# Kernel optimization log

Hardware: AMD Instinct MI355X
Metric: run time of the kernel (lower is better)

## Reference

```python
import jax, jax.numpy as jnp
import numpy as np

B, D_IN, D_OUT, DICT = 2048, 768, 768, 24576
TOP_K, TOP_K_AUX = 32, 512
L1_COEFF, AUX_PENALTY, N_DEAD = 0.001, 0.03125, 100.0


def setup_inputs() -> dict:
    key = jax.random.key(0)
    k1, k2, k3, k4, k5, k6 = jax.random.split(key, 6)
    x_in = jax.random.normal(k1, (B, D_IN), dtype=jnp.float32)
    y_target = jax.random.normal(k2, (B, D_OUT), dtype=jnp.float32)
    nb = jax.random.randint(k3, (DICT,), 0, 200).astype(jnp.float32)
    # kaiming-uniform-ish init
    bound_e = float(np.sqrt(6.0 / D_IN))
    W_enc = jax.random.uniform(k4, (D_IN, DICT), minval=-bound_e, maxval=bound_e, dtype=jnp.float32)
    bound_d = float(np.sqrt(6.0 / DICT))
    W_dec = jax.random.uniform(k5, (DICT, D_OUT), minval=-bound_d, maxval=bound_d, dtype=jnp.float32)
    W_dec = W_dec / jnp.linalg.norm(W_dec, axis=-1, keepdims=True)  # unit-norm rows
    b_dec = jnp.zeros((D_OUT,), dtype=jnp.float32)
    return {"x_in": x_in, "y_target": y_target, "num_batches_not_active": nb,
            "W_enc": W_enc, "W_dec": W_dec, "b_dec": b_dec}


def _unit_norm(x):
    m = x.mean(axis=-1, keepdims=True)
    x = x - m
    s = jnp.std(x, axis=-1, keepdims=True, ddof=1)  # torch .std is unbiased
    return x / (s + 1e-5), m, s


def reference(x_in, y_target, num_batches_not_active, W_enc, W_dec, b_dec):
    xn, _, _ = _unit_norm(x_in)
    yn, y_mean, y_std = _unit_norm(y_target)
    x_enc = xn - b_dec  # pre_enc_bias (input_size == output_size)
    acts = jax.nn.relu(x_enc @ W_enc)                      # [B, DICT]
    vals, idx = jax.lax.top_k(acts, TOP_K)                 # [B, TOP_K]
    rows = jnp.arange(B)[:, None]
    acts_sparse = jnp.zeros_like(acts).at[rows, idx].set(vals)
    y_pred = acts_sparse @ W_dec + b_dec                   # [B, D_OUT]
    y_pred_out = y_pred * y_std + y_mean

    # stateful dead-feature bookkeeping (update_inactive_features)
    col_active = acts_sparse.sum(axis=0) > 0
    nb = jnp.where(col_active, 0.0, num_batches_not_active + 1.0)

    l2_loss = jnp.mean((y_pred - yn) ** 2)
    l1_norm = jnp.mean(jnp.abs(acts_sparse).sum(axis=-1))
    l1_loss = L1_COEFF * l1_norm
    l0_norm = jnp.mean((acts_sparse > 0).astype(jnp.float32).sum(axis=-1))

    # auxiliary loss on dead features (static-shape masked top-k; masked cols
    # get -1 < relu acts so extras relu-clip to 0 -> same math as torch gather)
    dead = nb >= N_DEAD
    masked = jnp.where(dead[None, :], acts, -1.0)
    av, ai = jax.lax.top_k(masked, TOP_K_AUX)
    av = jax.nn.relu(av)
    acts_aux = jnp.zeros_like(acts).at[rows, ai].set(av)
    y_pred_aux = acts_aux @ W_dec
    residual = yn - y_pred
    l2_aux = AUX_PENALTY * jnp.mean((y_pred_aux - residual) ** 2)
    aux_loss = jnp.where(dead.any(), l2_aux, 0.0)

    loss = l2_loss + l1_loss + aux_loss
    num_dead_features = (nb > N_DEAD).sum()
    return (y_pred_out, acts_sparse, loss, l2_loss, l1_loss, l0_norm, l1_norm,
            aux_loss, num_dead_features)
```

## Files before the change

### kernel.cpp

```cpp
#include <hip/hip_runtime.h>
#include <math.h>

#define BATCH 2048
#define DIN 768
#define DICT 24576
#define KM 32
#define KA 512
#define NPT 48
#define L1_COEFF 0.001f
#define AUX_PENALTY 0.03125f
#define CAND_MAX 128
#define CAND_DELTA 0.08f
#define AUX_SPLIT 8

typedef __attribute__((ext_vector_type(8))) short bf16x8;
typedef __attribute__((ext_vector_type(8))) unsigned short u16x8;
typedef __attribute__((ext_vector_type(4))) float f32x4;

constexpr size_t WS_XENC   = 0;
constexpr size_t WS_YN     = WS_XENC + (size_t)BATCH*DIN;
constexpr size_t WS_YMEAN  = WS_YN + (size_t)BATCH*DIN;
constexpr size_t WS_YSTD   = WS_YMEAN + BATCH;
constexpr size_t WS_RES    = WS_YSTD + BATCH;
constexpr size_t WS_NSEL   = WS_RES + (size_t)BATCH*DIN;
constexpr size_t WS_SEL    = WS_NSEL + BATCH;
constexpr size_t WS_SELV   = WS_SEL + (size_t)BATCH*KM;
constexpr size_t WS_COLACT = WS_SELV + (size_t)BATCH*KM;
constexpr size_t WS_ACC    = WS_COLACT + DICT;
constexpr size_t WS_DB     = WS_ACC + 8;
constexpr size_t WS_XEB    = WS_DB + DICT/32;
constexpr size_t WS_WETF   = WS_XEB + (size_t)BATCH*DIN/2;
constexpr size_t WS_WETB   = WS_WETF + (size_t)DICT*DIN;
constexpr size_t WS_WDB    = WS_WETB + (size_t)DICT*DIN/2;
constexpr size_t WS_DCNT   = WS_XEB;
constexpr size_t WS_DPREF  = WS_XEB + DICT/32;
constexpr size_t WS_META   = WS_XEB + 2*(DICT/32);

__device__ __forceinline__ unsigned short f2b(float f){
    unsigned u = __float_as_uint(f);
    return (unsigned short)((u + 0x7fffu + ((u >> 16) & 1u)) >> 16);
}
__device__ __forceinline__ float b2f(unsigned short h){ return __uint_as_float(((unsigned)h) << 16); }

__device__ __forceinline__ void gld_lds16(const void* g, void* l){
    __builtin_amdgcn_global_load_lds(
        (const __attribute__((address_space(1))) unsigned int*)g,
        (__attribute__((address_space(3))) unsigned int*)l, 16, 0, 0);
}

__device__ __forceinline__ int blk_count512_w(int cw, int* s16, int par){
    if ((threadIdx.x & 63) == 0) s16[par*8 + (threadIdx.x >> 6)] = cw;
    __syncthreads();
    int tot = 0;
    #pragma unroll
    for (int w=0; w<8; w++) tot += s16[par*8+w];
    return tot;
}
__device__ __forceinline__ float blk_sum512(float v, float* s16, int par){
    #pragma unroll
    for (int off=32; off; off>>=1) v += __shfl_down(v, off);
    if ((threadIdx.x & 63) == 0) s16[par*8 + (threadIdx.x >> 6)] = v;
    __syncthreads();
    float t = 0.f;
    #pragma unroll
    for (int w=0; w<8; w++) t += s16[par*8+w];
    return t;
}
__device__ __forceinline__ float blk_sum256(float v, float* s8, int par){
    #pragma unroll
    for (int off=32; off; off>>=1) v += __shfl_down(v, off);
    if ((threadIdx.x & 63) == 0) s8[par*4 + (threadIdx.x >> 6)] = v;
    __syncthreads();
    float t = 0.f;
    #pragma unroll
    for (int w=0; w<4; w++) t += s8[par*4+w];
    return t;
}

__global__ __launch_bounds__(256) void normalize_k(const float* __restrict__ x,
        const float* __restrict__ y, const float* __restrict__ bdec,
        float* __restrict__ ws){
    __shared__ float s8[8];
    int b = blockIdx.x; bool isy = b >= BATCH; int row = isy ? b - BATCH : b;
    const float* src = (isy ? y : x) + (size_t)row*DIN;
    int tid = threadIdx.x;
    float v0 = src[tid], v1 = src[tid+256], v2 = src[tid+512];
    float s = blk_sum256(v0+v1+v2, s8, 0);
    float mean = s * (1.f/(float)DIN);
    float d0 = v0-mean, d1 = v1-mean, d2 = v2-mean;
    float vs = blk_sum256(d0*d0+d1*d1+d2*d2, s8, 1);
    float sd = sqrtf(vs / (float)(DIN-1));
    float inv = 1.f / (sd + 1e-5f);
    if (isy){
        float* yn = ws + WS_YN + (size_t)row*DIN;
        yn[tid] = d0*inv; yn[tid+256] = d1*inv; yn[tid+512] = d2*inv;
        if (tid==0){ ws[WS_YMEAN+row] = mean; ws[WS_YSTD+row] = sd; }
    } else {
        float* xe = ws + WS_XENC + (size_t)row*DIN;
        unsigned short* xeb = (unsigned short*)(ws + WS_XEB) + (size_t)row*DIN;
        float e0 = d0*inv - bdec[tid];
        float e1 = d1*inv - bdec[tid+256];
        float e2 = d2*inv - bdec[tid+512];
        xe[tid] = e0; xe[tid+256] = e1; xe[tid+512] = e2;
        xeb[tid] = f2b(e0); xeb[tid+256] = f2b(e1); xeb[tid+512] = f2b(e2);
    }
}

__global__ __launch_bounds__(256) void transpose_k(const float* __restrict__ W,
        float* __restrict__ Tf, unsigned short* __restrict__ Tb){
    __shared__ float t[32][33];
    int n0 = blockIdx.x*32, k0 = blockIdx.y*32;
    int r = threadIdx.x >> 5, c = threadIdx.x & 31;
    #pragma unroll
    for (int rr=r; rr<32; rr+=8) t[rr][c] = W[(size_t)(k0+rr)*DICT + n0 + c];
    __syncthreads();
    #pragma unroll
    for (int rr=r; rr<32; rr+=8){
        float v = t[c][rr];
        Tf[(size_t)(n0+rr)*DIN + k0 + c] = v;
        Tb[(size_t)(n0+rr)*DIN + k0 + c] = f2b(v);
    }
}

__global__ __launch_bounds__(256) void wdect_k(const float* __restrict__ W,
        unsigned short* __restrict__ T){
    __shared__ float t[32][33];
    int j0 = blockIdx.x*32, n0 = blockIdx.y*32;
    int r = threadIdx.x >> 5, c = threadIdx.x & 31;
    #pragma unroll
    for (int rr=r; rr<32; rr+=8) t[rr][c] = W[(size_t)(j0+rr)*DIN + n0 + c];
    __syncthreads();
    #pragma unroll
    for (int rr=r; rr<32; rr+=8)
        T[(size_t)(n0+rr)*DICT + j0 + c] = f2b(t[c][rr]);
}

__global__ __launch_bounds__(256) void gemm_mfma(const unsigned short* __restrict__ Abf,
        const unsigned short* __restrict__ Bbf, unsigned short* __restrict__ C){
    __shared__ __align__(16) unsigned short As[128*64];
    __shared__ __align__(16) unsigned short Bs[128*64];
    const int tid = threadIdx.x;
    const int w = tid >> 6, lane = tid & 63;
    const int m0 = blockIdx.y*128, n0 = blockIdx.x*128;
    const int srow = lane >> 3;
    const int schunk = (lane & 7) ^ srow;
    const int wm = (w >> 1)*64, wn = (w & 1)*64;
    f32x4 acc[16];
    #pragma unroll
    for (int i=0;i<16;i++) acc[i] = (f32x4){0.f,0.f,0.f,0.f};
    for (int kt = 0; kt < DIN; kt += 64){
        #pragma unroll
        for (int q=0;q<4;q++){
            int s = w*4 + q;
            int row = 8*s + srow;
            gld_lds16(Abf + (size_t)(m0+row)*DIN + kt + schunk*8, &As[8*s*64]);
            gld_lds16(Bbf + (size_t)(n0+row)*DIN + kt + schunk*8, &Bs[8*s*64]);
        }
        __syncthreads();
        #pragma unroll
        for (int kk=0; kk<64; kk+=32){
            bf16x8 af[4], bfr[4];
            int ch = (kk>>3) + (lane>>4);
            #pragma unroll
            for (int i=0;i<4;i++){
                int row = wm + i*16 + (lane&15);
                af[i] = *(const bf16x8*)&As[row*64 + ((ch ^ (row&7))<<3)];
            }
            #pragma unroll
            for (int j=0;j<4;j++){
                int row = wn + j*16 + (lane&15);
                bfr[j] = *(const bf16x8*)&Bs[row*64 + ((ch ^ (row&7))<<3)];
            }
            #pragma unroll
            for (int i=0;i<4;i++)
                #pragma unroll
                for (int j=0;j<4;j++)
                    acc[i*4+j] = __builtin_amdgcn_mfma_f32_16x16x32_bf16(af[i], bfr[j], acc[i*4+j], 0,0,0);
        }
        __syncthreads();
    }
    #pragma unroll
    for (int i=0;i<4;i++){
        #pragma unroll
        for (int r=0;r<4;r++){
            int m = m0 + wm + i*16 + (lane>>4)*4 + r;
            unsigned short* crow = C + (size_t)m*DICT + n0 + wn + (lane&15);
            #pragma unroll
            for (int j=0;j<4;j++)
                crow[j*16] = f2b(fmaxf(acc[i*4+j][r], 0.f) + 0.0f);
        }
    }
}

__global__ __launch_bounds__(512) void topk_main(const unsigned short* __restrict__ actsb,
        const float* __restrict__ WeTf, const float* __restrict__ Wdec,
        const float* __restrict__ bdec, float* __restrict__ ws,
        float* __restrict__ ypred_out){
    const int row = blockIdx.x, tid = threadIdx.x;
    const int lane = tid & 63, wid = tid >> 6;
    __shared__ int   s_i16[16];
    __shared__ float s_f16[16];
    __shared__ float s_x[DIN];
    __shared__ int   s_ci[CAND_MAX];
    __shared__ float s_cv[CAND_MAX];
    __shared__ int   s_li[KM];
    __shared__ float s_lv[KM];
    __shared__ int   s_n, s_m;
    const unsigned short* arow = actsb + (size_t)row * DICT;
    const float* xrow = ws + WS_XENC + (size_t)row * DIN;
    unsigned short h[NPT];
    #pragma unroll
    for (int i=0;i<6;i++){
        u16x8 v = *(const u16x8*)&arow[i*4096 + tid*8];
        #pragma unroll
        for (int e=0;e<8;e++) h[i*8+e] = v[e];
    }
    s_x[tid] = xrow[tid];
    if (tid < DIN-512) s_x[tid+512] = xrow[tid+512];
    if (tid == 0){ s_n = 0; s_m = 0; }

    int par = 0;
    unsigned prefix = 0;
    for (int bit=14; bit>=0; bit--){
        unsigned cand = prefix | (1u<<bit);
        int c = 0;
        #pragma unroll
        for (int q=0;q<NPT;q++) c += (int)__popcll(__ballot((unsigned)h[q] >= cand));
        int tot = blk_count512_w(c, s_i16, par); par ^= 1;
        if (tot >= KM) prefix = cand;
    }
    float tc = b2f((unsigned short)prefix) - CAND_DELTA;
    #pragma unroll
    for (int q=0;q<NPT;q++){
        if (b2f(h[q]) > tc){
            int p = atomicAdd(&s_n, 1);
            if (p < CAND_MAX) s_ci[p] = (q>>3)*4096 + tid*8 + (q&7);
        }
    }
    __syncthreads();
    int nc = s_n; if (nc > CAND_MAX) nc = CAND_MAX;
    for (int c = wid; c < nc; c += 8){
        const float* wr = WeTf + (size_t)s_ci[c]*DIN;
        float p = 0.f;
        #pragma unroll
        for (int t=0; t<12; t++) p = fmaf(s_x[lane + 64*t], wr[lane + 64*t], p);
        #pragma unroll
        for (int off=32; off; off>>=1) p += __shfl_down(p, off);
        if (lane == 0) s_cv[c] = fmaxf(p, 0.f);
    }
    __syncthreads();
    if (tid < nc){
        float vi = s_cv[tid]; int ii = s_ci[tid];
        int rank = 0;
        for (int j=0; j<nc; j++){
            float vj = s_cv[j];
            rank += (vj > vi) || (vj == vi && s_ci[j] < ii);
        }
        if (rank < KM){
            int p = atomicAdd(&s_m, 1);
            s_li[p] = ii; s_lv[p] = vi;
        }
    }
    __syncthreads();
    if (tid < KM){
        ((int*)ws)[WS_COLACT + s_li[tid]] = 1;
        ((int*)ws)[WS_SEL  + (size_t)row*KM + tid] = s_li[tid];
        ws[WS_SELV + (size_t)row*KM + tid] = s_lv[tid];
    }
    if (tid == 0){
        float l1 = 0.f; int l0 = 0;
        for (int l=0;l<KM;l++){ l1 += s_lv[l]; l0 += (s_lv[l] > 0.f); }
        atomicAdd(&ws[WS_ACC+1], l1);
        atomicAdd(&ws[WS_ACC+2], (float)l0);
    }
    __syncthreads();
    float ym = ws[WS_YMEAN+row], ys = ws[WS_YSTD+row];
    float l2loc = 0.f;
    for (int c = tid; c < DIN; c += 512){
        float acc = bdec[c];
        #pragma unroll 4
        for (int l=0;l<KM;l++) acc = fmaf(s_lv[l], Wdec[(size_t)s_li[l]*DIN + c], acc);
        float ynv = ws[WS_YN + (size_t)row*DIN + c];
        float d = acc - ynv;
        l2loc += d*d;
        ws[WS_RES + (size_t)row*DIN + c] = ynv - acc;
        ypred_out[(size_t)row*DIN + c] = fmaf(acc, ys, ym);
    }
    float l2t = blk_sum512(l2loc, s_f16, 0);
    if (tid==0) atomicAdd(&ws[WS_ACC+0], l2t);
}

__global__ __launch_bounds__(256) void dead_update(const float* __restrict__ nb,
        float* __restrict__ ws){
    int j = blockIdx.x*256 + threadIdx.x;
    int lane = threadIdx.x & 63;
    int act = ((const int*)ws)[WS_COLACT + j];
    float nbn = act ? 0.f : nb[j] + 1.f;
    bool dead = nbn >= 100.0f;
    unsigned long long bal = __ballot(dead ? 1 : 0);
    if (lane == 0){
        unsigned* db = (unsigned*)(ws + WS_DB);
        int* dc = (int*)(ws + WS_DCNT);
        int w = j >> 5;
        db[w]   = (unsigned)bal;
        db[w+1] = (unsigned)(bal >> 32);
        dc[w]   = __popc((unsigned)bal);
        dc[w+1] = __popc((unsigned)(bal >> 32));
        if (bal) atomicOr(((int*)ws) + WS_ACC + 5, 1);
    }
    int c = (nbn > 100.0f) ? 1 : 0;
    #pragma unroll
    for (int off=32; off; off>>=1) c += __shfl_down(c, off);
    if (lane == 0 && c) atomicAdd(&ws[WS_ACC+4], (float)c);
}

__global__ __launch_bounds__(256) void scan_k(float* __restrict__ ws){
    __shared__ int s[DICT/32];
    const int* dc = (const int*)(ws + WS_DCNT);
    int tid = threadIdx.x;
    for (int i=tid; i<DICT/32; i+=256) s[i] = dc[i];
    __syncthreads();
    for (int off=1; off<DICT/32; off<<=1){
        int v[3];
        #pragma unroll
        for (int k=0;k<3;k++){ int i = tid + 256*k; v[k] = (i >= off) ? s[i-off] : 0; }
        __syncthreads();
        #pragma unroll
        for (int k=0;k<3;k++){ int i = tid + 256*k; s[i] += v[k]; }
        __syncthreads();
    }
    int* dp = (int*)(ws + WS_DPREF);
    for (int i=tid; i<DICT/32; i+=256) dp[i] = s[i] - dc[i];
    if (tid == 0){
        int nd = s[DICT/32 - 1];
        int ndpad = (nd + 63) & ~63;
        int nkt = ndpad >> 6;
        int* meta = (int*)(ws + WS_META);
        meta[0] = nd; meta[1] = ndpad; meta[2] = nkt;
        meta[3] = (nkt + AUX_SPLIT - 1) / AUX_SPLIT;
    }
}

__global__ __launch_bounds__(256) void wdtcompact_k(float* __restrict__ ws,
        unsigned short* __restrict__ wdt){
    __shared__ unsigned s_db[DICT/32];
    __shared__ int      s_dp[DICT/32];
    const int tid = threadIdx.x, n = blockIdx.x;
    for (int i=tid; i<DICT/32; i+=256){
        s_db[i] = ((const unsigned*)(ws + WS_DB))[i];
        s_dp[i] = ((const int*)(ws + WS_DPREF))[i];
    }
    const int nd    = ((const int*)(ws + WS_META))[0];
    const int ndpad = ((const int*)(ws + WS_META))[1];
    __syncthreads();
    unsigned short* row = wdt + (size_t)n*DICT;
    for (int ch = 0; ch < DICT; ch += 4096){
        unsigned short v[16];
        u16x8 a = *(const u16x8*)&row[ch + tid*16];
        u16x8 b = *(const u16x8*)&row[ch + tid*16 + 8];
        #pragma unroll
        for (int e=0;e<8;e++){ v[e] = a[e]; v[8+e] = b[e]; }
        __syncthreads();
        int w = (ch>>5) + (tid>>1);
        unsigned dbw = s_db[w]; int dpw = s_dp[w];
        int bit0 = (tid&1)*16;
        #pragma unroll
        for (int e=0;e<16;e++){
            int bit = bit0 + e;
            if ((dbw >> bit) & 1u)
                row[dpw + __popc(dbw & ((1u<<bit)-1u))] = v[e];
        }
        __syncthreads();
    }
    for (int t = nd + tid; t < ndpad; t += 256) row[t] = 0;
}

__global__ __launch_bounds__(512) void aux_select(unsigned short* __restrict__ actsb,
        float* __restrict__ ws){
    const int row = blockIdx.x, tid = threadIdx.x;
    __shared__ int      s_i16[16];
    __shared__ unsigned s_db[DICT/32];
    __shared__ int      s_dp[DICT/32];
    unsigned short* arow = actsb + (size_t)row * DICT;
    for (int i=tid; i<DICT/32; i+=512){
        s_db[i] = ((const unsigned*)(ws + WS_DB))[i];
        s_dp[i] = ((const int*)(ws + WS_DPREF))[i];
    }
    const int nd    = ((const int*)(ws + WS_META))[0];
    const int ndpad = ((const int*)(ws + WS_META))[1];
    __syncthreads();

    unsigned short key[NPT];
    #pragma unroll
    for (int i=0;i<6;i++){
        u16x8 v = *(const u16x8*)&arow[i*4096 + tid*8];
        unsigned dbw = s_db[i*128 + (tid>>2)];
        #pragma unroll
        for (int e=0;e<8;e++){
            unsigned short hv = v[e];
            key[i*8+e] = (((dbw >> ((tid&3)*8 + e)) & 1u) && hv) ? hv : 0;
        }
    }

    int par = 0;
    unsigned prefix = 0;
    for (int bit=14; bit>=0; bit--){
        unsigned cand = prefix | (1u<<bit);
        int c = 0;
        #pragma unroll
        for (int q=0;q<NPT;q++) c += (int)__popcll(__ballot((unsigned)key[q] >= cand));
        int tot = blk_count512_w(c, s_i16, par); par ^= 1;
        if (tot >= KA) prefix = cand;
    }
    unsigned thr = prefix ? prefix : 1u;

    #pragma unroll
    for (int i=0;i<6;i++){
        int w = i*128 + (tid>>2);
        unsigned dbw = s_db[w];
        int dpw = s_dp[w];
        #pragma unroll
        for (int e=0;e<8;e++){
            int bit = (tid&3)*8 + e;
            if ((dbw >> bit) & 1u){
                int p = dpw + __popc(dbw & ((1u<<bit)-1u));
                unsigned short kv = key[i*8+e];
                arow[p] = ((unsigned)kv >= thr) ? kv : (unsigned short)0;
            }
        }
    }
    for (int t = nd + tid; t < ndpad; t += 512) arow[t] = 0;
}

__global__ __launch_bounds__(256) void aux_gemm(const unsigned short* __restrict__ Abf,
        const unsigned short* __restrict__ Bbf, const float* __restrict__ ws,
        float* __restrict__ yaux){
    const int nkt   = ((const int*)(ws + WS_META))[2];
    const int chunk = ((const int*)(ws + WS_META))[3];
    int t0 = blockIdx.z * chunk;
    int t1 = t0 + chunk; if (t1 > nkt) t1 = nkt;
    if (t0 >= t1) return;
    __shared__ __align__(16) unsigned short As[128*64];
    __shared__ __align__(16) unsigned short Bs[128*64];
    const int tid = threadIdx.x;
    const int w = tid >> 6, lane = tid & 63;
    const int m0 = blockIdx.y*128, n0 = blockIdx.x*128;
    const int srow = lane >> 3;
    const int schunk = (lane & 7) ^ srow;
    const int wm = (w >> 1)*64, wn = (w & 1)*64;
    f32x4 acc[16];
    #pragma unroll
    for (int i=0;i<16;i++) acc[i] = (f32x4){0.f,0.f,0.f,0.f};
    for (int t = t0; t < t1; ++t){
        int kt = t*64;
        #pragma unroll
        for (int q=0;q<4;q++){
            int s = w*4 + q;
            int row = 8*s + srow;
            gld_lds16(Abf + (size_t)(m0+row)*DICT + kt + schunk*8, &As[8*s*64]);
            gld_lds16(Bbf + (size_t)(n0+row)*DICT + kt + schunk*8, &Bs[8*s*64]);
        }
        __syncthreads();
        #pragma unroll
        for (int kk=0; kk<64; kk+=32){
            bf16x8 af[4], bfr[4];
            int ch = (kk>>3) + (lane>>4);
            #pragma unroll
            for (int i=0;i<4;i++){
                int row = wm + i*16 + (lane&15);
                af[i] = *(const bf16x8*)&As[row*64 + ((ch ^ (row&7))<<3)];
            }
            #pragma unroll
            for (int j=0;j<4;j++){
                int row = wn + j*16 + (lane&15);
                bfr[j] = *(const bf16x8*)&Bs[row*64 + ((ch ^ (row&7))<<3)];
            }
            #pragma unroll
            for (int i=0;i<4;i++)
                #pragma unroll
                for (int j=0;j<4;j++)
                    acc[i*4+j] = __builtin_amdgcn_mfma_f32_16x16x32_bf16(af[i], bfr[j], acc[i*4+j], 0,0,0);
        }
        __syncthreads();
    }
    #pragma unroll
    for (int i=0;i<4;i++){
        #pragma unroll
        for (int r=0;r<4;r++){
            int m = m0 + wm + i*16 + (lane>>4)*4 + r;
            float* crow = yaux + (size_t)m*DIN + n0 + wn + (lane&15);
            #pragma unroll
            for (int j=0;j<4;j++) atomicAdd(&crow[j*16], acc[i*4+j][r]);
        }
    }
}

__global__ __launch_bounds__(256) void auxloss_k(const float* __restrict__ yaux,
        float* __restrict__ ws){
    __shared__ float s8[8];
    const float4* y4 = (const float4*)yaux;
    const float4* r4 = (const float4*)(ws + WS_RES);
    float s = 0.f;
    const size_t n4 = (size_t)BATCH*DIN/4;
    for (size_t i = (size_t)blockIdx.x*256 + threadIdx.x; i < n4; i += (size_t)gridDim.x*256){
        float4 a = y4[i], b = r4[i];
        float d0 = a.x-b.x, d1 = a.y-b.y, d2 = a.z-b.z, d3 = a.w-b.w;
        s += d0*d0 + d1*d1 + d2*d2 + d3*d3;
    }
    float tot = blk_sum256(s, s8, 0);
    if (threadIdx.x == 0) atomicAdd(&ws[WS_ACC+3], tot);
}

__global__ __launch_bounds__(256) void zscatter(const float* __restrict__ ws,
        float* __restrict__ acts){
    const int row = blockIdx.x, tid = threadIdx.x;
    float4 z = make_float4(0.f,0.f,0.f,0.f);
    float4* arow4 = (float4*)(acts + (size_t)row*DICT);
    #pragma unroll
    for (int i=0;i<24;i++) arow4[tid + 256*i] = z;
    __syncthreads();
    if (tid < KM){
        int j   = ((const int*)ws)[WS_SEL + (size_t)row*KM + tid];
        float v = ws[WS_SELV + (size_t)row*KM + tid];
        (acts + (size_t)row*DICT)[j] = v;
    }
}

__global__ void finalize_k(const float* __restrict__ ws, float* __restrict__ out){
    if (threadIdx.x == 0){
        float l2   = ws[WS_ACC+0] / (float)((size_t)BATCH*DIN);
        float l1n  = ws[WS_ACC+1] / (float)BATCH;
        float l1l  = L1_COEFF * l1n;
        float l0   = ws[WS_ACC+2] / (float)BATCH;
        float auxm = AUX_PENALTY * (ws[WS_ACC+3] / (float)((size_t)BATCH*DIN));
        int any    = ((const int*)ws)[WS_ACC+5];
        float auxl = any ? auxm : 0.f;
        out[0] = l2 + l1l + auxl;
        out[1] = l2;
        out[2] = l1l;
        out[3] = l0;
        out[4] = l1n;
        out[5] = auxl;
        out[6] = ws[WS_ACC+4];
    }
}

extern "C" void kernel_launch(void* const* d_in, const int* in_sizes, int n_in,
                              void* d_out, int out_size, void* d_ws, size_t ws_size,
                              hipStream_t stream){
    const float* x_in = (const float*)d_in[0];
    const float* y_t  = (const float*)d_in[1];
    const float* nb   = (const float*)d_in[2];
    const float* Wenc = (const float*)d_in[3];
    const float* Wdec = (const float*)d_in[4];
    const float* bdec = (const float*)d_in[5];
    float* out  = (float*)d_out;
    float* ws   = (float*)d_ws;
    float* acts = out + (size_t)BATCH*DIN;
    float* scal = out + (size_t)BATCH*DIN + (size_t)BATCH*DICT;
    unsigned short* actsb = (unsigned short*)acts;

    unsigned short* xeb  = (unsigned short*)(ws + WS_XEB);
    float*          wetf = ws + WS_WETF;
    unsigned short* wetb = (unsigned short*)(ws + WS_WETB);
    unsigned short* wdt  = (unsigned short*)(ws + WS_WDB);
    float*          yaux = ws + WS_XENC;

    hipMemsetAsync(ws + WS_COLACT, 0, (DICT + 8) * sizeof(float), stream);
    normalize_k<<<2*BATCH, 256, 0, stream>>>(x_in, y_t, bdec, ws);
    transpose_k<<<dim3(DICT/32, DIN/32), 256, 0, stream>>>(Wenc, wetf, wetb);
    wdect_k<<<dim3(DICT/32, DIN/32), 256, 0, stream>>>(Wdec, wdt);
    gemm_mfma<<<dim3(DICT/128, BATCH/128), 256, 0, stream>>>(xeb, wetb, actsb);
    topk_main<<<BATCH, 512, 0, stream>>>(actsb, wetf, Wdec, bdec, ws, out);
    hipMemsetAsync(yaux, 0, (size_t)BATCH*DIN*sizeof(float), stream);
    dead_update<<<DICT/256, 256, 0, stream>>>(nb, ws);
    scan_k<<<1, 256, 0, stream>>>(ws);
    wdtcompact_k<<<DIN, 256, 0, stream>>>(ws, wdt);
    aux_select<<<BATCH, 512, 0, stream>>>(actsb, ws);
    aux_gemm<<<dim3(DIN/128, BATCH/128, AUX_SPLIT), 256, 0, stream>>>(actsb, wdt, ws, yaux);
    auxloss_k<<<256, 256, 0, stream>>>(yaux, ws);
    zscatter<<<BATCH, 256, 0, stream>>>(ws, acts);
    finalize_k<<<1, 64, 0, stream>>>(ws, scal);
}
```

Measured before the change: 855.6 us.

## Fuse transposes, dead-scan and aux-loss kernels; remap GEMM blocks for XCD locality

Merges the two weight-transpose kernels into one launch, folds dead-feature update and prefix scan into a single 768-thread block, and computes the aux loss inside the zero-scatter kernel so yaux is read per row there. It also linearizes the GEMM and aux GEMM grids and remaps block indices so blocks that share tiles land on the same XCD. The aim is fewer launches and better L2 reuse. The single-block dead scan serializes 24576 columns onto one CU.

```diff
diff --git a/kernel.cpp b/kernel.cpp
--- a/kernel.cpp
+++ b/kernel.cpp
@@ -32,7 +32,6 @@
 constexpr size_t WS_WETF   = WS_XEB + (size_t)BATCH*DIN/2;
 constexpr size_t WS_WETB   = WS_WETF + (size_t)DICT*DIN;
 constexpr size_t WS_WDB    = WS_WETB + (size_t)DICT*DIN/2;
-constexpr size_t WS_DCNT   = WS_XEB;
 constexpr size_t WS_DPREF  = WS_XEB + DICT/32;
 constexpr size_t WS_META   = WS_XEB + 2*(DICT/32);
 
@@ -106,33 +105,26 @@
     }
 }
 
-__global__ __launch_bounds__(256) void transpose_k(const float* __restrict__ W,
-        float* __restrict__ Tf, unsigned short* __restrict__ Tb){
-    __shared__ float t[32][33];
-    int n0 = blockIdx.x*32, k0 = blockIdx.y*32;
+__global__ __launch_bounds__(256) void transboth_k(const float* __restrict__ We,
+        const float* __restrict__ Wd, float* __restrict__ Tf,
+        unsigned short* __restrict__ Tb, unsigned short* __restrict__ Td){
+    __shared__ float t1[32][33];
+    __shared__ float t2[32][33];
+    int a0 = blockIdx.x*32, k0 = blockIdx.y*32;
     int r = threadIdx.x >> 5, c = threadIdx.x & 31;
     #pragma unroll
-    for (int rr=r; rr<32; rr+=8) t[rr][c] = W[(size_t)(k0+rr)*DICT + n0 + c];
-    __syncthreads();
-    #pragma unroll
     for (int rr=r; rr<32; rr+=8){
-        float v = t[c][rr];
-        Tf[(size_t)(n0+rr)*DIN + k0 + c] = v;
-        Tb[(size_t)(n0+rr)*DIN + k0 + c] = f2b(v);
-    }
-}
-
-__global__ __launch_bounds__(256) void wdect_k(const float* __restrict__ W,
-        unsigned short* __restrict__ T){
-    __shared__ float t[32][33];
-    int j0 = blockIdx.x*32, n0 = blockIdx.y*32;
-    int r = threadIdx.x >> 5, c = threadIdx.x & 31;
-    #pragma unroll
-    for (int rr=r; rr<32; rr+=8) t[rr][c] = W[(size_t)(j0+rr)*DIN + n0 + c];
-    __syncthreads();
-    #pragma unroll
-    for (int rr=r; rr<32; rr+=8)
-        T[(size_t)(n0+rr)*DICT + j0 + c] = f2b(t[c][rr]);
+        t1[rr][c] = We[(size_t)(k0+rr)*DICT + a0 + c];
+        t2[rr][c] = Wd[(size_t)(a0+rr)*DIN + k0 + c];
+    }
+    __syncthreads();
+    #pragma unroll
+    for (int rr=r; rr<32; rr+=8){
+        float v = t1[c][rr];
+        Tf[(size_t)(a0+rr)*DIN + k0 + c] = v;
+        Tb[(size_t)(a0+rr)*DIN + k0 + c] = f2b(v);
+        Td[(size_t)(k0+rr)*DICT + a0 + c] = f2b(t2[c][rr]);
+    }
 }
 
 __global__ __launch_bounds__(256) void gemm_mfma(const unsigned short* __restrict__ Abf,
@@ -141,7 +133,12 @@
     __shared__ __align__(16) unsigned short Bs[128*64];
     const int tid = threadIdx.x;
     const int w = tid >> 6, lane = tid & 63;
-    const int m0 = blockIdx.y*128, n0 = blockIdx.x*128;
+    const int g = blockIdx.x;
+    const int xcd = g & 7;
+    const int s_ = g >> 3;
+    const int m_t = s_ & 15;
+    const int n_t = xcd + 8*(s_ >> 4);
+    const int m0 = m_t*128, n0 = n_t*128;
     const int srow = lane >> 3;
     const int schunk = (lane & 7) ^ srow;
     const int wm = (w >> 1)*64, wn = (w & 1)*64;
@@ -290,54 +287,46 @@
     if (tid==0) atomicAdd(&ws[WS_ACC+0], l2t);
 }
 
-__global__ __launch_bounds__(256) void dead_update(const float* __restrict__ nb,
+__global__ __launch_bounds__(768) void deadscan_k(const float* __restrict__ nb,
         float* __restrict__ ws){
-    int j = blockIdx.x*256 + threadIdx.x;
-    int lane = threadIdx.x & 63;
-    int act = ((const int*)ws)[WS_COLACT + j];
-    float nbn = act ? 0.f : nb[j] + 1.f;
-    bool dead = nbn >= 100.0f;
-    unsigned long long bal = __ballot(dead ? 1 : 0);
-    if (lane == 0){
-        unsigned* db = (unsigned*)(ws + WS_DB);
-        int* dc = (int*)(ws + WS_DCNT);
-        int w = j >> 5;
-        db[w]   = (unsigned)bal;
-        db[w+1] = (unsigned)(bal >> 32);
-        dc[w]   = __popc((unsigned)bal);
-        dc[w+1] = __popc((unsigned)(bal >> 32));
-        if (bal) atomicOr(((int*)ws) + WS_ACC + 5, 1);
-    }
-    int c = (nbn > 100.0f) ? 1 : 0;
-    #pragma unroll
-    for (int off=32; off; off>>=1) c += __shfl_down(c, off);
-    if (lane == 0 && c) atomicAdd(&ws[WS_ACC+4], (float)c);
-}
-
-__global__ __launch_bounds__(256) void scan_k(float* __restrict__ ws){
     __shared__ int s[DICT/32];
-    const int* dc = (const int*)(ws + WS_DCNT);
-    int tid = threadIdx.x;
-    for (int i=tid; i<DICT/32; i+=256) s[i] = dc[i];
+    __shared__ int c12[12];
+    const int t = threadIdx.x;
+    const int* colact = (const int*)ws + WS_COLACT;
+    unsigned bits = 0; int cgt = 0;
+    const int base = t*32;
+    #pragma unroll 8
+    for (int b=0;b<32;b++){
+        int j = base + b;
+        float nbn = colact[j] ? 0.f : nb[j] + 1.f;
+        bits |= (nbn >= 100.f ? 1u : 0u) << b;
+        cgt  += (nbn > 100.f) ? 1 : 0;
+    }
+    ((unsigned*)(ws + WS_DB))[t] = bits;
+    int pc = __popc(bits);
+    s[t] = pc;
+    #pragma unroll
+    for (int off=32; off; off>>=1) cgt += __shfl_down(cgt, off);
+    if ((t & 63) == 0) c12[t >> 6] = cgt;
     __syncthreads();
     for (int off=1; off<DICT/32; off<<=1){
-        int v[3];
-        #pragma unroll
-        for (int k=0;k<3;k++){ int i = tid + 256*k; v[k] = (i >= off) ? s[i-off] : 0; }
-        __syncthreads();
-        #pragma unroll
-        for (int k=0;k<3;k++){ int i = tid + 256*k; s[i] += v[k]; }
-        __syncthreads();
-    }
-    int* dp = (int*)(ws + WS_DPREF);
-    for (int i=tid; i<DICT/32; i+=256) dp[i] = s[i] - dc[i];
-    if (tid == 0){
-        int nd = s[DICT/32 - 1];
+        int v = (t >= off) ? s[t-off] : 0;
+        __syncthreads();
+        s[t] += v;
+        __syncthreads();
+    }
+    ((int*)(ws + WS_DPREF))[t] = s[t] - pc;
+    if (t == DICT/32 - 1){
+        int nd = s[t];
         int ndpad = (nd + 63) & ~63;
-        int nkt = ndpad >> 6;
         int* meta = (int*)(ws + WS_META);
-        meta[0] = nd; meta[1] = ndpad; meta[2] = nkt;
-        meta[3] = (nkt + AUX_SPLIT - 1) / AUX_SPLIT;
+        meta[0] = nd; meta[1] = ndpad; meta[2] = ndpad >> 6;
+        meta[3] = ((ndpad >> 6) + AUX_SPLIT - 1) / AUX_SPLIT;
+        int tot = 0;
+        #pragma unroll
+        for (int wv=0; wv<12; wv++) tot += c12[wv];
+        ws[WS_ACC+4] = (float)tot;
+        ((int*)ws)[WS_ACC+5] = (nd > 0) ? 1 : 0;
     }
 }
 
@@ -437,14 +426,19 @@
         float* __restrict__ yaux){
     const int nkt   = ((const int*)(ws + WS_META))[2];
     const int chunk = ((const int*)(ws + WS_META))[3];
-    int t0 = blockIdx.z * chunk;
+    const int g = blockIdx.x;
+    const int z = g & 7;
+    const int s_ = g >> 3;
+    const int m_t = s_ & 15;
+    const int n_t = s_ >> 4;
+    int t0 = z * chunk;
     int t1 = t0 + chunk; if (t1 > nkt) t1 = nkt;
     if (t0 >= t1) return;
     __shared__ __align__(16) unsigned short As[128*64];
     __shared__ __align__(16) unsigned short Bs[128*64];
     const int tid = threadIdx.x;
     const int w = tid >> 6, lane = tid & 63;
-    const int m0 = blockIdx.y*128, n0 = blockIdx.x*128;
+    const int m0 = m_t*128, n0 = n_t*128;
     const int srow = lane >> 3;
     const int schunk = (lane & 7) ^ srow;
     const int wm = (w >> 1)*64, wn = (w & 1)*64;
@@ -495,29 +489,23 @@
     }
 }
 
-__global__ __launch_bounds__(256) void auxloss_k(const float* __restrict__ yaux,
-        float* __restrict__ ws){
+__global__ __launch_bounds__(256) void zscatter(float* __restrict__ ws,
+        float* __restrict__ acts, const float* __restrict__ yaux){
     __shared__ float s8[8];
-    const float4* y4 = (const float4*)yaux;
-    const float4* r4 = (const float4*)(ws + WS_RES);
+    const int row = blockIdx.x, tid = threadIdx.x;
     float s = 0.f;
-    const size_t n4 = (size_t)BATCH*DIN/4;
-    for (size_t i = (size_t)blockIdx.x*256 + threadIdx.x; i < n4; i += (size_t)gridDim.x*256){
-        float4 a = y4[i], b = r4[i];
+    if (tid < DIN/4){
+        float4 a = ((const float4*)(yaux + (size_t)row*DIN))[tid];
+        float4 b = ((const float4*)(ws + WS_RES + (size_t)row*DIN))[tid];
         float d0 = a.x-b.x, d1 = a.y-b.y, d2 = a.z-b.z, d3 = a.w-b.w;
-        s += d0*d0 + d1*d1 + d2*d2 + d3*d3;
-    }
-    float tot = blk_sum256(s, s8, 0);
-    if (threadIdx.x == 0) atomicAdd(&ws[WS_ACC+3], tot);
-}
-
-__global__ __launch_bounds__(256) void zscatter(const float* __restrict__ ws,
-        float* __restrict__ acts){
-    const int row = blockIdx.x, tid = threadIdx.x;
+        s = d0*d0 + d1*d1 + d2*d2 + d3*d3;
+    }
     float4 z = make_float4(0.f,0.f,0.f,0.f);
     float4* arow4 = (float4*)(acts + (size_t)row*DICT);
     #pragma unroll
     for (int i=0;i<24;i++) arow4[tid + 256*i] = z;
+    float tot = blk_sum256(s, s8, 0);
+    if (tid == 0) atomicAdd(&ws[WS_ACC+3], tot);
     __syncthreads();
     if (tid < KM){
         int j   = ((const int*)ws)[WS_SEL + (size_t)row*KM + tid];
@@ -568,17 +556,14 @@
 
     hipMemsetAsync(ws + WS_COLACT, 0, (DICT + 8) * sizeof(float), stream);
     normalize_k<<<2*BATCH, 256, 0, stream>>>(x_in, y_t, bdec, ws);
-    transpose_k<<<dim3(DICT/32, DIN/32), 256, 0, stream>>>(Wenc, wetf, wetb);
-    wdect_k<<<dim3(DICT/32, DIN/32), 256, 0, stream>>>(Wdec, wdt);
-    gemm_mfma<<<dim3(DICT/128, BATCH/128), 256, 0, stream>>>(xeb, wetb, actsb);
+    transboth_k<<<dim3(DICT/32, DIN/32), 256, 0, stream>>>(Wenc, Wdec, wetf, wetb, wdt);
+    gemm_mfma<<<(DICT/128)*(BATCH/128), 256, 0, stream>>>(xeb, wetb, actsb);
     topk_main<<<BATCH, 512, 0, stream>>>(actsb, wetf, Wdec, bdec, ws, out);
     hipMemsetAsync(yaux, 0, (size_t)BATCH*DIN*sizeof(float), stream);
-    dead_update<<<DICT/256, 256, 0, stream>>>(nb, ws);
-    scan_k<<<1, 256, 0, stream>>>(ws);
+    deadscan_k<<<1, DICT/32, 0, stream>>>(nb, ws);
     wdtcompact_k<<<DIN, 256, 0, stream>>>(ws, wdt);
     aux_select<<<BATCH, 512, 0, stream>>>(actsb, ws);
-    aux_gemm<<<dim3(DIN/128, BATCH/128, AUX_SPLIT), 256, 0, stream>>>(actsb, wdt, ws, yaux);
-    auxloss_k<<<256, 256, 0, stream>>>(yaux, ws);
-    zscatter<<<BATCH, 256, 0, stream>>>(ws, acts);
+    aux_gemm<<<(DIN/128)*(BATCH/128)*AUX_SPLIT, 256, 0, stream>>>(actsb, wdt, ws, yaux);
+    zscatter<<<BATCH, 256, 0, stream>>>(ws, acts, yaux);
     finalize_k<<<1, 64, 0, stream>>>(ws, scal);
 }
```

Measured after the change: 866.4 us. About the same (+1.3%).
